# Kernel tuning notes

Measured on AMD Instinct MI355X. Metric: run time of the kernel, lower is better.

Reference implementation:

```python
import jax, jax.numpy as jnp
import numpy as np

N = 50000      # nodes
E = 800000     # edges (before self loops)
H = 2          # attention heads
CH = 64        # per-head hidden channels
IN = 128       # input features
OUT = 64       # output channels
EPS = 1e-5     # batchnorm eps
SLOPE = 0.2    # LeakyReLU negative slope


def _gat_conv(x, src, dst, W, a_src, a_dst, b, concat):
    # x: [N, Fin]; W: [Fin, H*C]; a_src/a_dst: [H, C]
    n = x.shape[0]
    h = (x @ W).reshape(n, H, -1)                       # [N, H, C]
    al_s = (h * a_src).sum(-1)                          # [N, H]
    al_d = (h * a_dst).sum(-1)                          # [N, H]
    e = al_s[src] + al_d[dst]                           # [E, H]
    e = jnp.where(e > 0, e, SLOPE * e)                  # LeakyReLU
    # softmax over edges grouped by destination node
    m = jax.ops.segment_max(e, dst, num_segments=n)
    ex = jnp.exp(e - m[dst])
    den = jax.ops.segment_sum(ex, dst, num_segments=n)
    alpha = ex / (den[dst] + 1e-16)                     # [E, H]
    out = jax.ops.segment_sum(h[src] * alpha[:, :, None], dst, num_segments=n)
    out = out.reshape(n, -1) if concat else out.mean(axis=1)
    return out + b


def _batchnorm(x, g, be):
    mu = x.mean(axis=0)
    var = x.var(axis=0)  # biased, as torch BN uses in training
    return (x - mu) * jax.lax.rsqrt(var + EPS) * g + be


def setup_inputs() -> dict:
    key = jax.random.key(0)
    ks = jax.random.split(key, 18)
    s = 0.1
    inp = {
        "x": jax.random.normal(ks[0], (N, IN), jnp.float32),
        "edge_index": jax.random.randint(ks[1], (2, E), 0, N, jnp.int64),
        # layer 0: IN -> H*CH (concat)
        "W0": jax.random.normal(ks[2], (IN, H * CH), jnp.float32) * s,
        "a_src0": jax.random.normal(ks[3], (H, CH), jnp.float32) * s,
        "a_dst0": jax.random.normal(ks[4], (H, CH), jnp.float32) * s,
        "b0": jnp.zeros((H * CH,), jnp.float32),
        "g0": jnp.ones((H * CH,), jnp.float32),
        "be0": jnp.zeros((H * CH,), jnp.float32),
        # layer 1: H*CH -> H*CH (concat)
        "W1": jax.random.normal(ks[5], (H * CH, H * CH), jnp.float32) * s,
        "a_src1": jax.random.normal(ks[6], (H, CH), jnp.float32) * s,
        "a_dst1": jax.random.normal(ks[7], (H, CH), jnp.float32) * s,
        "b1": jnp.zeros((H * CH,), jnp.float32),
        "g1": jnp.ones((H * CH,), jnp.float32),
        "be1": jnp.zeros((H * CH,), jnp.float32),
        # layer 2: H*CH -> OUT, concat=False (mean over heads)
        "W2": jax.random.normal(ks[8], (H * CH, H * OUT), jnp.float32) * s,
        "a_src2": jax.random.normal(ks[9], (H, OUT), jnp.float32) * s,
        "a_dst2": jax.random.normal(ks[10], (H, OUT), jnp.float32) * s,
        "b2": jnp.zeros((OUT,), jnp.float32),
    }
    return inp


def reference(x, edge_index, W0, a_src0, a_dst0, b0, g0, be0,
              W1, a_src1, a_dst1, b1, g1, be1,
              W2, a_src2, a_dst2, b2):
    # add self loops (PyG GATConv default)
    loop = jnp.arange(N, dtype=edge_index.dtype)
    src = jnp.concatenate([edge_index[0], loop])
    dst = jnp.concatenate([edge_index[1], loop])

    h = _gat_conv(x, src, dst, W0, a_src0, a_dst0, b0, concat=True)
    h = jax.nn.relu(_batchnorm(h, g0, be0))
    # dropout: eval mode (identity)
    h = _gat_conv(h, src, dst, W1, a_src1, a_dst1, b1, concat=True)
    h = jax.nn.relu(_batchnorm(h, g1, be1))
    out = _gat_conv(h, src, dst, W2, a_src2, a_dst2, b2, concat=False)
    return out
```

## Files before the change

### kernel.cpp

```cpp
#include <hip/hip_runtime.h>


#define N_NODES 50000
#define N_EDGES 800000
#define ET (N_EDGES + N_NODES)
#define FDIM 128
#define SLOPE 0.2f
#define BN_EPS 1e-5f
#define SCAN_NB 196
#define NRANGE 8
#define RNODES (N_NODES / NRANGE)
#define SCAT_SUB 128
#define SCAT_CH ((ET + SCAT_SUB - 1) / SCAT_SUB)

typedef __attribute__((ext_vector_type(8))) short bf16x8;
typedef __attribute__((ext_vector_type(4))) float f32x4;
typedef __attribute__((ext_vector_type(8))) unsigned short u16x8;

__device__ __forceinline__ unsigned short f2bf(float f) {
  unsigned u = __float_as_uint(f);
  u = u + 0x7fffu + ((u >> 16) & 1u);
  return (unsigned short)(u >> 16);
}
__device__ __forceinline__ float bflo(unsigned p) { return __uint_as_float(p << 16); }
__device__ __forceinline__ float bfhi(unsigned p) { return __uint_as_float(p & 0xffff0000u); }


__global__ __launch_bounds__(256) void hist_kernel(const int* __restrict__ dst,
                                                   int* __restrict__ counts) {
  int r = blockIdx.x & (NRANGE - 1);
  int s = blockIdx.x >> 3;
  int lo = r * RNODES, hi = lo + RNODES;
  int e0 = s * SCAT_CH;
  int e1 = e0 + SCAT_CH; if (e1 > ET) e1 = ET;
  for (int i = e0 + threadIdx.x; i < e1; i += 256) {
    int d = (i < N_EDGES) ? dst[i] : i - N_EDGES;
    if (d >= lo && d < hi) atomicAdd(&counts[d], 1);
  }
}

__global__ __launch_bounds__(256) void scan_blk(const int* __restrict__ counts,
                                                int* __restrict__ rowptr,
                                                int* __restrict__ partials) {
  int i = blockIdx.x * 256 + threadIdx.x;
  int lane = threadIdx.x & 63, wv = threadIdx.x >> 6;
  int c = (i < N_NODES) ? counts[i] : 0;
  int v = c;
#pragma unroll
  for (int off = 1; off < 64; off <<= 1) {
    int u = __shfl_up(v, off);
    if (lane >= off) v += u;
  }
  __shared__ int wsum[4];
  if (lane == 63) wsum[wv] = v;
  __syncthreads();
  int add = 0;
  for (int w = 0; w < wv; ++w) add += wsum[w];
  if (i < N_NODES) rowptr[i] = v - c + add;
  if (threadIdx.x == 255) partials[blockIdx.x] = add + v;
}

__global__ __launch_bounds__(256) void scan_top(int* __restrict__ partials) {
  int t = threadIdx.x;
  int lane = t & 63, wv = t >> 6;
  int c = (t < SCAN_NB) ? partials[t] : 0;
  int v = c;
#pragma unroll
  for (int off = 1; off < 64; off <<= 1) {
    int u = __shfl_up(v, off);
    if (lane >= off) v += u;
  }
  __shared__ int wsum[4];
  if (lane == 63) wsum[wv] = v;
  __syncthreads();
  int add = 0;
  for (int w = 0; w < wv; ++w) add += wsum[w];
  if (t < SCAN_NB) partials[t] = v - c + add;
}

__global__ __launch_bounds__(256) void scan_fin(int* __restrict__ rowptr,
                                                const int* __restrict__ partials,
                                                int* __restrict__ fill) {
  int i = blockIdx.x * 256 + threadIdx.x;
  if (i >= N_NODES) return;
  int v = rowptr[i] + partials[blockIdx.x];
  rowptr[i] = v;
  fill[i] = v;
  if (i == 0) rowptr[N_NODES] = ET;
}

__global__ __launch_bounds__(256) void scatter_kernel(const int* __restrict__ src,
                                                      const int* __restrict__ dst,
                                                      int* __restrict__ fill,
                                                      int* __restrict__ csr_src) {
  int r = blockIdx.x & (NRANGE - 1);
  int s = blockIdx.x >> 3;
  int lo = r * RNODES, hi = lo + RNODES;
  int e0 = s * SCAT_CH;
  int e1 = e0 + SCAT_CH; if (e1 > ET) e1 = ET;
  for (int i = e0 + threadIdx.x; i < e1; i += 256) {
    int d = (i < N_EDGES) ? dst[i] : i - N_EDGES;
    if (d >= lo && d < hi) {
      int sv = (i < N_EDGES) ? src[i] : d;
      int pos = atomicAdd(&fill[d], 1);
      csr_src[pos] = sv;
    }
  }
}

__global__ __launch_bounds__(256) void repack_w(const float* __restrict__ W0,
                                                const float* __restrict__ W1,
                                                const float* __restrict__ W2,
                                                unsigned short* __restrict__ Wr) {
  int i = blockIdx.x * 256 + threadIdx.x;
  if (i >= 3 * 16384) return;
  int L = i >> 14, rem = i & 16383;
  int t  = rem >> 11;
  int ks = (rem >> 9) & 3;
  int ln = (rem >> 3) & 63;
  int j  = rem & 7;
  int k   = ks * 32 + (ln >> 4) * 8 + j;
  int col = t * 16 + (ln & 15);
  const float* W = (L == 0) ? W0 : ((L == 1) ? W1 : W2);
  Wr[i] = f2bf(W[k * 128 + col]);
}

__global__ __launch_bounds__(256) void gemm_mfma(const float* __restrict__ Xin,
                                                 const unsigned short* __restrict__ WrL,
                                                 const float* __restrict__ part,
                                                 const float* __restrict__ g,
                                                 const float* __restrict__ be,
                                                 const float* __restrict__ a_src,
                                                 const float* __restrict__ a_dst,
                                                 unsigned short* __restrict__ Hbf,
                                                 float* __restrict__ als,
                                                 float* __restrict__ ald,
                                                 int doBN) {
  __shared__ unsigned short lds[4][16][128];
  __shared__ float ls_scale[128], ls_shift[128];
  int lane = threadIdx.x & 63;
  int wv   = threadIdx.x >> 6;

  if (doBN) {
    int t = threadIdx.x;
    if (t < 128) {
      float s = 0.f, q = 0.f;
#pragma unroll
      for (int k = 0; k < 32; ++k) {
        s += part[k * 256 + t];
        q += part[k * 256 + 128 + t];
      }
      float mu  = s * (1.f / N_NODES);
      float var = q * (1.f / N_NODES) - mu * mu;
      float sc  = rsqrtf(var + BN_EPS) * g[t];
      ls_scale[t] = sc;
      ls_shift[t] = be[t] - mu * sc;
    }
    __syncthreads();
  }

  int row0 = blockIdx.x * 64 + wv * 16;
  int gidx = lane & 15;
  int quad = lane >> 4;
  int rA   = row0 + gidx;
  int rAc  = rA < N_NODES ? rA : N_NODES - 1;
  int koff = quad * 8;

  f32x4 acc[8] = {};
#pragma unroll
  for (int ks = 0; ks < 4; ++ks) {
    int cb = ks * 32 + koff;
    const float4* xr = (const float4*)(Xin + (size_t)rAc * FDIM + cb);
    float4 xa = xr[0], xb = xr[1];
    float xv[8] = {xa.x, xa.y, xa.z, xa.w, xb.x, xb.y, xb.z, xb.w};
    bf16x8 afrag;
    if (doBN) {
#pragma unroll
      for (int j = 0; j < 8; ++j) {
        int c = cb + j;
        float v = fmaf(xv[j], ls_scale[c], ls_shift[c]);
        v = v > 0.f ? v : 0.f;
        afrag[j] = (short)f2bf(v);
      }
    } else {
#pragma unroll
      for (int j = 0; j < 8; ++j) afrag[j] = (short)f2bf(xv[j]);
    }
#pragma unroll
    for (int t = 0; t < 8; ++t) {
      bf16x8 bfrag = *(const bf16x8*)(WrL + ((size_t)((t * 4 + ks) * 64 + lane)) * 8);
      acc[t] = __builtin_amdgcn_mfma_f32_16x16x32_bf16(afrag, bfrag, acc[t], 0, 0, 0);
    }
  }

  float vs[2][4] = {}, vd[2][4] = {};
#pragma unroll
  for (int t = 0; t < 8; ++t) {
    int col = t * 16 + gidx;
    float as = a_src[col], ad = a_dst[col];
    int hd = t >> 2;
#pragma unroll
    for (int r = 0; r < 4; ++r) {
      vs[hd][r] = fmaf(acc[t][r], as, vs[hd][r]);
      vd[hd][r] = fmaf(acc[t][r], ad, vd[hd][r]);
    }
  }
#pragma unroll
  for (int off = 1; off < 16; off <<= 1) {
#pragma unroll
    for (int hd = 0; hd < 2; ++hd)
#pragma unroll
      for (int r = 0; r < 4; ++r) {
        vs[hd][r] += __shfl_xor(vs[hd][r], off);
        vd[hd][r] += __shfl_xor(vd[hd][r], off);
      }
  }
  if (gidx == 0) {
#pragma unroll
    for (int r = 0; r < 4; ++r) {
      int row = row0 + quad * 4 + r;
      if (row < N_NODES) {
        als[row * 2 + 0] = vs[0][r]; als[row * 2 + 1] = vs[1][r];
        ald[row * 2 + 0] = vd[0][r]; ald[row * 2 + 1] = vd[1][r];
      }
    }
  }

#pragma unroll
  for (int t = 0; t < 8; ++t)
#pragma unroll
    for (int r = 0; r < 4; ++r)
      lds[wv][quad * 4 + r][t * 16 + gidx] = f2bf(acc[t][r]);
  __syncthreads();
#pragma unroll
  for (int it = 0; it < 4; ++it) {
    int rloc = it * 4 + quad;
    int row = row0 + rloc;
    if (row < N_NODES)
      *(u16x8*)(Hbf + (size_t)row * FDIM + gidx * 8) = *(u16x8*)&lds[wv][rloc][gidx * 8];
  }
}

__global__ __launch_bounds__(256) void fused_agg(const int* __restrict__ rowptr,
                                                 const int* __restrict__ csr_src,
                                                 const unsigned* __restrict__ H2,
                                                 const float* __restrict__ als,
                                                 const float* __restrict__ ald,
                                                 float* __restrict__ A,
                                                 float* __restrict__ out,
                                                 const float* __restrict__ b2,
                                                 float* __restrict__ part,
                                                 int mode) {
  int lane = threadIdx.x & 63;
  bool hi = lane >= 32;
  int n = __builtin_amdgcn_readfirstlane((blockIdx.x * 256 + threadIdx.x) >> 6);
  int beg = rowptr[n], end = rowptr[n + 1];
  float2 adv = ((const float2*)ald)[n];
  float advh = hi ? adv.y : adv.x;

  int b0 = end - 4; if (b0 > beg) b0 = beg; if (b0 < 0) b0 = 0;
  int delta = beg - b0;
  int s0 = csr_src[b0], s1 = csr_src[b0 + 1], s2 = csr_src[b0 + 2], s3 = csr_src[b0 + 3];
  float2 A0 = ((const float2*)als)[s0];
  float2 A1 = ((const float2*)als)[s1];
  float2 A2 = ((const float2*)als)[s2];
  float2 A3 = ((const float2*)als)[s3];
  unsigned h0 = H2[(size_t)s0 * 64 + lane];
  unsigned h1 = H2[(size_t)s1 * 64 + lane];
  unsigned h2 = H2[(size_t)s2 * 64 + lane];
  unsigned h3 = H2[(size_t)s3 * 64 + lane];

  float l = 0.f, ox = 0.f, oy = 0.f;

#define STEP(AL, HH) { \
    float v_ = (hi ? AL.y : AL.x) + advh; \
    v_ = fmaxf(v_, SLOPE * v_); \
    float e_ = __expf(v_); \
    l += e_; \
    ox = fmaf(e_, bflo(HH), ox); \
    oy = fmaf(e_, bfhi(HH), oy); }

  int j = beg;
  for (; j + 4 <= end; j += 4) {
    int p = j + 4;
    int pp = p; if (pp > end - 4) pp = end - 4;
    int t0 = csr_src[pp], t1 = csr_src[pp + 1], t2 = csr_src[pp + 2], t3 = csr_src[pp + 3];
    float2 B0 = ((const float2*)als)[t0];
    float2 B1 = ((const float2*)als)[t1];
    float2 B2 = ((const float2*)als)[t2];
    float2 B3 = ((const float2*)als)[t3];
    unsigned g0 = H2[(size_t)t0 * 64 + lane];
    unsigned g1 = H2[(size_t)t1 * 64 + lane];
    unsigned g2 = H2[(size_t)t2 * 64 + lane];
    unsigned g3 = H2[(size_t)t3 * 64 + lane];

    STEP(A0, h0); STEP(A1, h1); STEP(A2, h2); STEP(A3, h3);

    delta = p - pp;
    A0 = B0; A1 = B1; A2 = B2; A3 = B3;
    h0 = g0; h1 = g1; h2 = g2; h3 = g3;
  }
  int rem = end - j;
  int hi_k = delta + rem;
  if (0 >= delta && 0 < hi_k) STEP(A0, h0);
  if (1 >= delta && 1 < hi_k) STEP(A1, h1);
  if (2 >= delta && 2 < hi_k) STEP(A2, h2);
  if (3 >= delta && 3 < hi_k) STEP(A3, h3);
#undef STEP

  float inv = 1.f / (l + 1e-16f);
  ox *= inv; oy *= inv;

  if (mode == 0) {
    float2 outv = {ox, oy};
    *(float2*)(A + (size_t)n * FDIM + lane * 2) = outv;
    __shared__ float sh[4][4][64];
    int wv = threadIdx.x >> 6;
    sh[wv][0][lane] = ox;
    sh[wv][1][lane] = oy;
    sh[wv][2][lane] = ox * ox;
    sh[wv][3][lane] = oy * oy;
    __syncthreads();
    if (threadIdx.x < 64) {
      int t = threadIdx.x;
      float a0 = 0.f, a1 = 0.f, a2 = 0.f, a3 = 0.f;
#pragma unroll
      for (int w = 0; w < 4; ++w) {
        a0 += sh[w][0][t]; a1 += sh[w][1][t];
        a2 += sh[w][2][t]; a3 += sh[w][3][t];
      }
      float* slot = part + (blockIdx.x & 31) * 256;
      atomicAdd(&slot[2 * t],           a0);
      atomicAdd(&slot[2 * t + 1],       a1);
      atomicAdd(&slot[128 + 2 * t],     a2);
      atomicAdd(&slot[128 + 2 * t + 1], a3);
    }
  } else {
    float px = __shfl_xor(ox, 32);
    float py = __shfl_xor(oy, 32);
    if (lane < 32) {
      int c = lane * 2;
      float2 outv = {0.5f * (ox + px) + b2[c], 0.5f * (oy + py) + b2[c + 1]};
      *(float2*)(out + (size_t)n * 64 + c) = outv;
    }
  }
}

extern "C" void kernel_launch(void* const* d_in, const int* in_sizes, int n_in,
                              void* d_out, int out_size, void* d_ws, size_t ws_size,
                              hipStream_t stream) {
  const float* x  = (const float*)d_in[0];
  const int*   ei = (const int*)d_in[1];
  const int* src = ei;
  const int* dst = ei + N_EDGES;

  const float* W[3]    = {(const float*)d_in[2],  (const float*)d_in[8],  (const float*)d_in[14]};
  const float* asrc[3] = {(const float*)d_in[3],  (const float*)d_in[9],  (const float*)d_in[15]};
  const float* adst[3] = {(const float*)d_in[4],  (const float*)d_in[10], (const float*)d_in[16]};
  const float* g[2]    = {(const float*)d_in[6],  (const float*)d_in[12]};
  const float* be[2]   = {(const float*)d_in[7],  (const float*)d_in[13]};
  const float* b2      = (const float*)d_in[17];

  int*   counts   = (int*)d_ws;
  int*   rowptr   = counts + 50048;
  int*   fill     = rowptr + 50048;
  int*   partials = fill + 50048;
  int*   csr_src  = partials + 256;
  float* part     = (float*)(csr_src + 850048);
  float* als      = part + 8192;
  float* ald      = als + 100096;
  unsigned short* Wr  = (unsigned short*)(ald + 100096);
  unsigned short* Hbf = Wr + 3 * 16384;
  float* A        = (float*)(Hbf + (size_t)N_NODES * FDIM);

  hipMemsetAsync(counts, 0, (size_t)N_NODES * sizeof(int), stream);
  hist_kernel<<<NRANGE * SCAT_SUB, 256, 0, stream>>>(dst, counts);
  scan_blk<<<SCAN_NB, 256, 0, stream>>>(counts, rowptr, partials);
  scan_top<<<1, 256, 0, stream>>>(partials);
  scan_fin<<<SCAN_NB, 256, 0, stream>>>(rowptr, partials, fill);
  scatter_kernel<<<NRANGE * SCAT_SUB, 256, 0, stream>>>(src, dst, fill, csr_src);
  repack_w<<<(3 * 16384 + 255) / 256, 256, 0, stream>>>(W[0], W[1], W[2], Wr);

  const int gemm_grid = (N_NODES + 63) / 64;
  const int agg_grid  = N_NODES * 64 / 256;

  for (int L = 0; L < 3; ++L) {
    const float* fin = (L == 0) ? x : A;
    int doBN = (L > 0);
    const float* gg = doBN ? g[L - 1]  : (const float*)nullptr;
    const float* bb = doBN ? be[L - 1] : (const float*)nullptr;
    gemm_mfma<<<gemm_grid, 256, 0, stream>>>(fin, Wr + (size_t)L * 16384, part, gg, bb,
                                             asrc[L], adst[L], Hbf, als, ald, doBN);
    if (L < 2)
      hipMemsetAsync(part, 0, 8192 * sizeof(float), stream);
    fused_agg<<<agg_grid, 256, 0, stream>>>(rowptr, csr_src, (const unsigned*)Hbf,
                                            als, ald, A, (float*)d_out, b2, part,
                                            (L == 2) ? 2 : 0);
  }
}
```

Measured before the change: 360.7 us.

## Build CSR via per-edge atomic rank and store intermediate activations as bf16

Measured after the change: 345.1 us. 4.3% less time.

```diff
diff --git a/kernel.cpp b/kernel.cpp
--- a/kernel.cpp
+++ b/kernel.cpp
@@ -8,10 +8,6 @@
 #define SLOPE 0.2f
 #define BN_EPS 1e-5f
 #define SCAN_NB 196
-#define NRANGE 8
-#define RNODES (N_NODES / NRANGE)
-#define SCAT_SUB 128
-#define SCAT_CH ((ET + SCAT_SUB - 1) / SCAT_SUB)
 
 typedef __attribute__((ext_vector_type(8))) short bf16x8;
 typedef __attribute__((ext_vector_type(4))) float f32x4;
@@ -26,17 +22,13 @@
 __device__ __forceinline__ float bfhi(unsigned p) { return __uint_as_float(p & 0xffff0000u); }
 
 
-__global__ __launch_bounds__(256) void hist_kernel(const int* __restrict__ dst,
-                                                   int* __restrict__ counts) {
-  int r = blockIdx.x & (NRANGE - 1);
-  int s = blockIdx.x >> 3;
-  int lo = r * RNODES, hi = lo + RNODES;
-  int e0 = s * SCAT_CH;
-  int e1 = e0 + SCAT_CH; if (e1 > ET) e1 = ET;
-  for (int i = e0 + threadIdx.x; i < e1; i += 256) {
-    int d = (i < N_EDGES) ? dst[i] : i - N_EDGES;
-    if (d >= lo && d < hi) atomicAdd(&counts[d], 1);
-  }
+__global__ __launch_bounds__(256) void hist_rank(const int* __restrict__ dst,
+                                                 int* __restrict__ counts,
+                                                 int* __restrict__ rank) {
+  int i = blockIdx.x * 256 + threadIdx.x;
+  if (i >= ET) return;
+  int d = (i < N_EDGES) ? dst[i] : i - N_EDGES;
+  rank[i] = atomicAdd(&counts[d], 1);
 }
 
 __global__ __launch_bounds__(256) void scan_blk(const int* __restrict__ counts,
@@ -79,33 +71,23 @@
 }
 
 __global__ __launch_bounds__(256) void scan_fin(int* __restrict__ rowptr,
-                                                const int* __restrict__ partials,
-                                                int* __restrict__ fill) {
+                                                const int* __restrict__ partials) {
   int i = blockIdx.x * 256 + threadIdx.x;
   if (i >= N_NODES) return;
-  int v = rowptr[i] + partials[blockIdx.x];
-  rowptr[i] = v;
-  fill[i] = v;
+  rowptr[i] += partials[blockIdx.x];
   if (i == 0) rowptr[N_NODES] = ET;
 }
 
-__global__ __launch_bounds__(256) void scatter_kernel(const int* __restrict__ src,
-                                                      const int* __restrict__ dst,
-                                                      int* __restrict__ fill,
-                                                      int* __restrict__ csr_src) {
-  int r = blockIdx.x & (NRANGE - 1);
-  int s = blockIdx.x >> 3;
-  int lo = r * RNODES, hi = lo + RNODES;
-  int e0 = s * SCAT_CH;
-  int e1 = e0 + SCAT_CH; if (e1 > ET) e1 = ET;
-  for (int i = e0 + threadIdx.x; i < e1; i += 256) {
-    int d = (i < N_EDGES) ? dst[i] : i - N_EDGES;
-    if (d >= lo && d < hi) {
-      int sv = (i < N_EDGES) ? src[i] : d;
-      int pos = atomicAdd(&fill[d], 1);
-      csr_src[pos] = sv;
-    }
-  }
+__global__ __launch_bounds__(256) void scatter_pos(const int* __restrict__ src,
+                                                   const int* __restrict__ dst,
+                                                   const int* __restrict__ rowptr,
+                                                   const int* __restrict__ rank,
+                                                   int* __restrict__ csr_src) {
+  int i = blockIdx.x * 256 + threadIdx.x;
+  if (i >= ET) return;
+  int d, s;
+  if (i < N_EDGES) { d = dst[i]; s = src[i]; } else { d = s = i - N_EDGES; }
+  csr_src[rowptr[d] + rank[i]] = s;
 }
 
 __global__ __launch_bounds__(256) void repack_w(const float* __restrict__ W0,
@@ -125,7 +107,7 @@
   Wr[i] = f2bf(W[k * 128 + col]);
 }
 
-__global__ __launch_bounds__(256) void gemm_mfma(const float* __restrict__ Xin,
+__global__ __launch_bounds__(256) void gemm_mfma(const void* __restrict__ Xin,
                                                  const unsigned short* __restrict__ WrL,
                                                  const float* __restrict__ part,
                                                  const float* __restrict__ g,
@@ -135,13 +117,13 @@
                                                  unsigned short* __restrict__ Hbf,
                                                  float* __restrict__ als,
                                                  float* __restrict__ ald,
-                                                 int doBN) {
+                                                 int inBF) {
   __shared__ unsigned short lds[4][16][128];
   __shared__ float ls_scale[128], ls_shift[128];
   int lane = threadIdx.x & 63;
   int wv   = threadIdx.x >> 6;
 
-  if (doBN) {
+  if (inBF) {
     int t = threadIdx.x;
     if (t < 128) {
       float s = 0.f, q = 0.f;
@@ -170,11 +152,22 @@
 #pragma unroll
   for (int ks = 0; ks < 4; ++ks) {
     int cb = ks * 32 + koff;
-    const float4* xr = (const float4*)(Xin + (size_t)rAc * FDIM + cb);
-    float4 xa = xr[0], xb = xr[1];
-    float xv[8] = {xa.x, xa.y, xa.z, xa.w, xb.x, xb.y, xb.z, xb.w};
+    float xv[8];
+    if (inBF) {
+      const uint4* xr = (const uint4*)((const unsigned*)Xin + (size_t)rAc * 64 + (cb >> 1));
+      uint4 xa = *xr;
+      xv[0] = bflo(xa.x); xv[1] = bfhi(xa.x);
+      xv[2] = bflo(xa.y); xv[3] = bfhi(xa.y);
+      xv[4] = bflo(xa.z); xv[5] = bfhi(xa.z);
+      xv[6] = bflo(xa.w); xv[7] = bfhi(xa.w);
+    } else {
+      const float4* xr = (const float4*)((const float*)Xin + (size_t)rAc * FDIM + cb);
+      float4 xa = xr[0], xb = xr[1];
+      xv[0] = xa.x; xv[1] = xa.y; xv[2] = xa.z; xv[3] = xa.w;
+      xv[4] = xb.x; xv[5] = xb.y; xv[6] = xb.z; xv[7] = xb.w;
+    }
     bf16x8 afrag;
-    if (doBN) {
+    if (inBF) {
 #pragma unroll
       for (int j = 0; j < 8; ++j) {
         int c = cb + j;
@@ -246,7 +239,7 @@
                                                  const unsigned* __restrict__ H2,
                                                  const float* __restrict__ als,
                                                  const float* __restrict__ ald,
-                                                 float* __restrict__ A,
+                                                 unsigned* __restrict__ Abf,
                                                  float* __restrict__ out,
                                                  const float* __restrict__ b2,
                                                  float* __restrict__ part,
@@ -312,8 +305,8 @@
   ox *= inv; oy *= inv;
 
   if (mode == 0) {
-    float2 outv = {ox, oy};
-    *(float2*)(A + (size_t)n * FDIM + lane * 2) = outv;
+    unsigned pack = ((unsigned)f2bf(oy) << 16) | (unsigned)f2bf(ox);
+    Abf[(size_t)n * 64 + lane] = pack;
     __shared__ float sh[4][4][64];
     int wv = threadIdx.x >> 6;
     sh[wv][0][lane] = ox;
@@ -363,38 +356,38 @@
 
   int*   counts   = (int*)d_ws;
   int*   rowptr   = counts + 50048;
-  int*   fill     = rowptr + 50048;
-  int*   partials = fill + 50048;
-  int*   csr_src  = partials + 256;
+  int*   partials = rowptr + 50048;
+  int*   rank     = partials + 256;
+  int*   csr_src  = rank + 850048;
   float* part     = (float*)(csr_src + 850048);
   float* als      = part + 8192;
   float* ald      = als + 100096;
   unsigned short* Wr  = (unsigned short*)(ald + 100096);
   unsigned short* Hbf = Wr + 3 * 16384;
-  float* A        = (float*)(Hbf + (size_t)N_NODES * FDIM);
+  unsigned* Abf   = (unsigned*)(Hbf + (size_t)N_NODES * FDIM);
 
   hipMemsetAsync(counts, 0, (size_t)N_NODES * sizeof(int), stream);
-  hist_kernel<<<NRANGE * SCAT_SUB, 256, 0, stream>>>(dst, counts);
+  hist_rank<<<(ET + 255) / 256, 256, 0, stream>>>(dst, counts, rank);
   scan_blk<<<SCAN_NB, 256, 0, stream>>>(counts, rowptr, partials);
   scan_top<<<1, 256, 0, stream>>>(partials);
-  scan_fin<<<SCAN_NB, 256, 0, stream>>>(rowptr, partials, fill);
-  scatter_kernel<<<NRANGE * SCAT_SUB, 256, 0, stream>>>(src, dst, fill, csr_src);
+  scan_fin<<<SCAN_NB, 256, 0, stream>>>(rowptr, partials);
+  scatter_pos<<<(ET + 255) / 256, 256, 0, stream>>>(src, dst, rowptr, rank, csr_src);
   repack_w<<<(3 * 16384 + 255) / 256, 256, 0, stream>>>(W[0], W[1], W[2], Wr);
 
   const int gemm_grid = (N_NODES + 63) / 64;
   const int agg_grid  = N_NODES * 64 / 256;
 
   for (int L = 0; L < 3; ++L) {
-    const float* fin = (L == 0) ? x : A;
-    int doBN = (L > 0);
-    const float* gg = doBN ? g[L - 1]  : (const float*)nullptr;
-    const float* bb = doBN ? be[L - 1] : (const float*)nullptr;
+    const void* fin = (L == 0) ? (const void*)x : (const void*)Abf;
+    int inBF = (L > 0);
+    const float* gg = inBF ? g[L - 1]  : (const float*)nullptr;
+    const float* bb = inBF ? be[L - 1] : (const float*)nullptr;
     gemm_mfma<<<gemm_grid, 256, 0, stream>>>(fin, Wr + (size_t)L * 16384, part, gg, bb,
-                                             asrc[L], adst[L], Hbf, als, ald, doBN);
+                                             asrc[L], adst[L], Hbf, als, ald, inBF);
     if (L < 2)
       hipMemsetAsync(part, 0, 8192 * sizeof(float), stream);
     fused_agg<<<agg_grid, 256, 0, stream>>>(rowptr, csr_src, (const unsigned*)Hbf,
-                                            als, ald, A, (float*)d_out, b2, part,
+                                            als, ald, Abf, (float*)d_out, b2, part,
                                             (L == 2) ? 2 : 0);
   }
 }
```
